# Optimization experiments

Measured on AMD Instinct MI355X. Metric: run time of the kernel, lower is better.

## Reference

```python
import math
import jax, jax.numpy as jnp
import numpy as np

NUM_HEADS = 16
HEAD_DIM = 128
CTX = 4096

def _rope_tables(head_dim, context_length, theta_base=10000.0):
    inv_freq = 1.0 / (theta_base ** (np.arange(0, head_dim, 2)[: head_dim // 2].astype(np.float32) / head_dim))
    pos = np.arange(context_length, dtype=np.float32)
    ang = pos[:, None] * inv_freq[None, :]
    ang = np.concatenate([ang, ang], axis=1)  # [ctx, head_dim]
    return jnp.asarray(np.cos(ang), jnp.float32), jnp.asarray(np.sin(ang), jnp.float32)

def _apply_rope(x, cos, sin):
    # x: [b, h, s, d]
    s, d = x.shape[2], x.shape[3]
    x1, x2 = x[..., : d // 2], x[..., d // 2 :]
    rotated = jnp.concatenate([-x2, x1], axis=-1)
    c = cos[:s][None, None]
    sn = sin[:s][None, None]
    return x * c + rotated * sn

def setup_inputs() -> dict:
    key = jax.random.key(0)
    kx, kq, kk, kv, ko = jax.random.split(key, 5)
    B, S, H = 2, 2048, 2048
    scale = 1.0 / math.sqrt(H)
    x = jax.random.normal(kx, (B, S, H), jnp.float32)
    Wq = jax.random.normal(kq, (H, H), jnp.float32) * scale
    Wk = jax.random.normal(kk, (H, H), jnp.float32) * scale
    Wv = jax.random.normal(kv, (H, H), jnp.float32) * scale
    Wo = jax.random.normal(ko, (H, H), jnp.float32) * scale
    cos, sin = _rope_tables(HEAD_DIM, CTX)
    return {"x": x, "Wq": Wq, "Wk": Wk, "Wv": Wv, "Wo": Wo, "cos": cos, "sin": sin}

def reference(x, Wq, Wk, Wv, Wo, cos, sin):
    B, S, Hd = x.shape
    nh, hd = NUM_HEADS, HEAD_DIM
    # nn.Linear(no bias): y = x @ W.T
    q = jnp.einsum('bsh,oh->bso', x, Wq).reshape(B, S, nh, hd).transpose(0, 2, 1, 3)
    k = jnp.einsum('bsh,oh->bso', x, Wk).reshape(B, S, nh, hd).transpose(0, 2, 1, 3)
    v = jnp.einsum('bsh,oh->bso', x, Wv).reshape(B, S, nh, hd).transpose(0, 2, 1, 3)
    q = _apply_rope(q, cos, sin)
    k = _apply_rope(k, cos, sin)
    # NOTE: faithful to source bug: scores are divided by (1/sqrt(d)),
    # i.e. MULTIPLIED by sqrt(head_dim).
    scores = jnp.einsum('bhqd,bhkd->bhqk', q, k) * math.sqrt(hd)
    causal = jnp.triu(jnp.ones((S, S), bool), k=1)
    scores = jnp.where(causal[None, None], -jnp.inf, scores)
    attn = jax.nn.softmax(scores, axis=-1)
    ctx = jnp.einsum('bhqk,bhkd->bhqd', attn, v)
    ctx = ctx.transpose(0, 2, 1, 3).reshape(B, S, Hd)
    return jnp.einsum('bsh,oh->bso', ctx, Wo)
```

## Files before the change

kernel.cpp:

```cpp
#include <hip/hip_runtime.h>

typedef unsigned short u16;
typedef __attribute__((ext_vector_type(8))) _Float16 f16x8;
typedef __attribute__((ext_vector_type(4))) float f32x4;

#define S_CTX 2048
#define DMODEL 2048

#define WAITVM(N) asm volatile("s_waitcnt vmcnt(" #N ")" ::: "memory")
#define SBAR() __builtin_amdgcn_s_barrier()

__device__ __forceinline__ u16 f2h(float f) {
  _Float16 h = (_Float16)f; u16 u; __builtin_memcpy(&u, &h, 2); return u;
}
__device__ __forceinline__ float h2f(u16 u) {
  _Float16 h; __builtin_memcpy(&h, &u, 2); return (float)h;
}
__device__ __forceinline__ void gload16(const u16* g, u16* l) {
  __builtin_amdgcn_global_load_lds(
      (const __attribute__((address_space(1))) unsigned int*)g,
      (__attribute__((address_space(3))) unsigned int*)l, 16, 0, 0);
}

__global__ void split_all(const float* __restrict__ x, const float* __restrict__ Wq,
                          const float* __restrict__ Wk, const float* __restrict__ Wv,
                          const float* __restrict__ Wo,
                          u16* xh, u16* xl, u16* Wqh, u16* Wql,
                          u16* Wkh, u16* Wkl, u16* Wvh, u16* Woh) {
  size_t i = (size_t)blockIdx.x * 256 + threadIdx.x;
  const size_t NX = 8388608, NW = 4194304;
  if (i < NX) {
    float v = x[i];
    u16 h = f2h(v);
    xh[i] = h; xl[i] = f2h(v - h2f(h));
  } else {
    size_t j = i - NX;
    int wsel = (int)(j >> 22);
    size_t o = j & (NW - 1);
    if (wsel == 0) { float v = Wq[o] * 64.f; u16 h = f2h(v); Wqh[o] = h; Wql[o] = f2h(v - h2f(h)); }
    else if (wsel == 1) { float v = Wk[o] * 64.f; u16 h = f2h(v); Wkh[o] = h; Wkl[o] = f2h(v - h2f(h)); }
    else if (wsel == 2) { Wvh[o] = f2h(Wv[o] * 64.f); }
    else { Woh[o] = f2h(Wo[o] * 64.f); }
  }
}

template <int NT, int MODE>
__device__ __forceinline__ void gemm_core(
    u16* sm, const u16* __restrict__ Am, const u16* __restrict__ Alm,
    const u16* __restrict__ Bm, const u16* __restrict__ Blm,
    float* __restrict__ Cf, u16* __restrict__ Ch,
    const float* __restrict__ cosT, const float* __restrict__ sinT,
    int N, int K, int m0, int n0, float oscale) {
  const int tid = threadIdx.x;
  const int w = tid >> 6, lane = tid & 63;
  const int quad = lane >> 4, l16 = lane & 15;
  const int wm = (w >> 1) << 6, wn = (w & 1) << 6;
  const int lrow = lane >> 2, lcol = (lane & 3) << 3;
  const int lcs = lcol ^ (((lrow >> 1) & 3) << 3);
  const int qsw = (quad << 3) ^ (((l16 >> 1) & 3) << 3);

  auto stageH = [&](int bufb, int k0) {
#pragma unroll
    for (int j = 0; j < 2; ++j) {
      int r = w * 32 + j * 16 + lrow;
      int lb = bufb + (w * 32 + j * 16) * 32;
      size_t ga = (size_t)(m0 + r) * K + k0 + lcs;
      size_t gb = (size_t)(n0 + r) * K + k0 + lcs;
      gload16(Am + ga, &sm[lb]);
      gload16(Bm + gb, &sm[lb + 4096]);
    }
  };
  auto stageL = [&](int bufb, int k0) {
#pragma unroll
    for (int j = 0; j < 2; ++j) {
      int r = w * 32 + j * 16 + lrow;
      int lb = bufb + (w * 32 + j * 16) * 32;
      size_t ga = (size_t)(m0 + r) * K + k0 + lcs;
      size_t gb = (size_t)(n0 + r) * K + k0 + lcs;
      gload16(Blm + gb, &sm[lb + 8192]);
      gload16(Alm + ga, &sm[lb + 12288]);
    }
  };

  f32x4 acc[4][4];
#pragma unroll
  for (int i = 0; i < 4; ++i)
#pragma unroll
    for (int n = 0; n < 4; ++n) acc[i][n] = (f32x4){0.f, 0.f, 0.f, 0.f};

  const int NTL = K >> 5;

  if (NT == 3) {
    stageH(0, 0);
    stageL(0, 0);
    for (int t = 0; t < NTL; ++t) {
      const int cur = (t & 1) << 14;
      const int nxt = 16384 - cur;
      const int k0n = (t + 1) << 5;
      const bool more = (t + 1 < NTL);

      WAITVM(4);
      SBAR();
      f16x8 ah[4], bh[4];
#pragma unroll
      for (int i = 0; i < 4; ++i)
        ah[i] = *(const f16x8*)&sm[cur + (wm + i * 16 + l16) * 32 + qsw];
#pragma unroll
      for (int n = 0; n < 4; ++n)
        bh[n] = *(const f16x8*)&sm[cur + 4096 + (wn + n * 16 + l16) * 32 + qsw];
      if (more) stageH(nxt, k0n);
#pragma unroll
      for (int i = 0; i < 4; ++i)
#pragma unroll
        for (int n = 0; n < 4; ++n)
          acc[i][n] = __builtin_amdgcn_mfma_f32_16x16x32_f16(ah[i], bh[n], acc[i][n], 0, 0, 0);

      if (more) { WAITVM(4); } else { WAITVM(0); }
      SBAR();
      f16x8 bl[4], al[4];
#pragma unroll
      for (int n = 0; n < 4; ++n)
        bl[n] = *(const f16x8*)&sm[cur + 8192 + (wn + n * 16 + l16) * 32 + qsw];
#pragma unroll
      for (int i = 0; i < 4; ++i)
        al[i] = *(const f16x8*)&sm[cur + 12288 + (wm + i * 16 + l16) * 32 + qsw];
      if (more) stageL(nxt, k0n);
#pragma unroll
      for (int i = 0; i < 4; ++i)
#pragma unroll
        for (int n = 0; n < 4; ++n) {
          acc[i][n] = __builtin_amdgcn_mfma_f32_16x16x32_f16(ah[i], bl[n], acc[i][n], 0, 0, 0);
          acc[i][n] = __builtin_amdgcn_mfma_f32_16x16x32_f16(al[i], bh[n], acc[i][n], 0, 0, 0);
        }
    }
  } else {
    stageH(0, 0);
    stageH(8192, 32);
    for (int t = 0; t < NTL; ++t) {
      const int cur = (t % 3) * 8192;
      if (t + 1 < NTL) { WAITVM(4); } else { WAITVM(0); }
      SBAR();
      f16x8 ah[4], bh[4];
#pragma unroll
      for (int i = 0; i < 4; ++i)
        ah[i] = *(const f16x8*)&sm[cur + (wm + i * 16 + l16) * 32 + qsw];
#pragma unroll
      for (int n = 0; n < 4; ++n)
        bh[n] = *(const f16x8*)&sm[cur + 4096 + (wn + n * 16 + l16) * 32 + qsw];
      if (t + 2 < NTL) stageH(((t + 2) % 3) * 8192, (t + 2) << 5);
#pragma unroll
      for (int i = 0; i < 4; ++i)
#pragma unroll
        for (int n = 0; n < 4; ++n)
          acc[i][n] = __builtin_amdgcn_mfma_f32_16x16x32_f16(ah[i], bh[n], acc[i][n], 0, 0, 0);
    }
  }

  if (MODE == 3) {
    float* fs = (float*)sm;
    const int p = w >> 1;
#pragma unroll
    for (int i = 0; i < 4; ++i) {
      __syncthreads();
#pragma unroll
      for (int n = 0; n < 4; ++n)
#pragma unroll
        for (int r = 0; r < 4; ++r)
          fs[p * 2048 + (quad * 4 + r) * 128 + wn + n * 16 + l16] = acc[i][n][r];
      __syncthreads();
#pragma unroll
      for (int n = 0; n < 4; ++n) {
        const int col = wn + n * 16 + l16;
        const int cc = col ^ 64;
        const float sgn = (col < 64) ? -1.f : 1.f;
#pragma unroll
        for (int r = 0; r < 4; ++r) {
          const int row16 = quad * 4 + r;
          const int grow = m0 + wm + i * 16 + row16;
          const int s = grow & (S_CTX - 1);
          const float c = cosT[s * 128 + col];
          const float sn = sinT[s * 128 + col];
          const float x = fs[p * 2048 + row16 * 128 + col];
          const float xp = fs[p * 2048 + row16 * 128 + cc];
          Ch[(size_t)grow * N + n0 + col] = f2h((x * c + sgn * xp * sn) * oscale);
        }
      }
    }
    return;
  }
#pragma unroll
  for (int i = 0; i < 4; ++i)
#pragma unroll
    for (int n = 0; n < 4; ++n) {
      const int row0 = m0 + wm + i * 16 + quad * 4;
      const int col = n0 + wn + n * 16 + l16;
      if (MODE == 0) {
#pragma unroll
        for (int r = 0; r < 4; ++r) Cf[(size_t)(row0 + r) * N + col] = acc[i][n][r] * oscale;
      } else {
        int brow = row0 >> 11, s0 = row0 & 2047;
        int hh = col >> 7, d = col & 127;
        ushort4 pk;
        pk.x = f2h(acc[i][n][0]);
        pk.y = f2h(acc[i][n][1]);
        pk.z = f2h(acc[i][n][2]);
        pk.w = f2h(acc[i][n][3]);
        *(ushort4*)(Ch + ((size_t)(brow * 16 + hh) * 128 + d) * 2048 + s0) = pk;
      }
    }
}

__global__ __launch_bounds__(256) void qkv_kernel(
    const u16* __restrict__ xh, const u16* __restrict__ xl,
    const u16* __restrict__ Wqh, const u16* __restrict__ Wql,
    const u16* __restrict__ Wkh, const u16* __restrict__ Wkl,
    const u16* __restrict__ Wvh,
    const float* __restrict__ cosT, const float* __restrict__ sinT,
    u16* qh, u16* kh, u16* vt) {
  __shared__ u16 sm[32768];
  const int m0 = blockIdx.y << 7, n0 = blockIdx.x << 7;
  const float qs = 0.002762135864009951f;
  if (blockIdx.z == 0)
    gemm_core<3, 3>(sm, xh, xl, Wqh, Wql, nullptr, qh, cosT, sinT, DMODEL, DMODEL, m0, n0, qs);
  else if (blockIdx.z == 1)
    gemm_core<3, 3>(sm, xh, xl, Wkh, Wkl, nullptr, kh, cosT, sinT, DMODEL, DMODEL, m0, n0, 1.f);
  else
    gemm_core<1, 2>(sm, xh, nullptr, Wvh, nullptr, nullptr, vt, nullptr, nullptr, DMODEL, DMODEL, m0, n0, 1.f);
}

__global__ __launch_bounds__(256) void out_kernel(
    const u16* __restrict__ ch, const u16* __restrict__ Woh, float* __restrict__ out) {
  __shared__ u16 sm[24576];
  gemm_core<1, 0>(sm, ch, nullptr, Woh, nullptr, out, nullptr, nullptr, nullptr, DMODEL, DMODEL,
                  blockIdx.y << 7, blockIdx.x << 7, 1.f / 4096.f);
}

__global__ __launch_bounds__(512, 4) void attn_kernel(
    const u16* __restrict__ Qh, const u16* __restrict__ Kh,
    const u16* __restrict__ VT, u16* __restrict__ Ch) {
  const int lin = blockIdx.x | (blockIdx.y << 4);
  const int pair = lin & 255;
  const int bh = pair >> 3;
  const int q8 = pair & 7;
  const int qt = (lin < 256) ? (15 - q8) : q8;
  const int b = bh >> 4, h = bh & 15;
  const int tid = threadIdx.x;
  const int w = tid >> 6, lane = tid & 63;
  const int quad = lane >> 4, l16 = lane & 15;

  __shared__ u16 sKh[64 * 136];
  __shared__ u16 sVt[128 * 72];
  __shared__ u16 sPb[8 * 1088];
  u16* sP = &sPb[w * 1088];

  const size_t bhbase = (size_t)b * S_CTX * DMODEL + (size_t)h * 128;
  const size_t vtbase = (size_t)bh * 128 * 2048;

  int kr[2], kc[2], vr[2], vc[2];
#pragma unroll
  for (int j = 0; j < 2; ++j) {
    int c = j * 512 + tid;
    kr[j] = c >> 4; kc[j] = (c & 15) << 3;
    vr[j] = c >> 3; vc[j] = (c & 7) << 3;
  }

  const int qr0 = qt * 128 + w * 16;
  const size_t qoff = bhbase + (size_t)(qr0 + l16) * DMODEL;
  f16x8 qf[4];
#pragma unroll
  for (int c = 0; c < 4; ++c) qf[c] = *(const f16x8*)(Qh + qoff + c * 32 + quad * 8);

  f32x4 oacc[8];
#pragma unroll
  for (int d = 0; d < 8; ++d) oacc[d] = (f32x4){0.f, 0.f, 0.f, 0.f};
  float m_r = -INFINITY;
  float l_r = 0.f;

  f16x8 rkh[2], rvt[2];
#pragma unroll
  for (int j = 0; j < 2; ++j) {
    rkh[j] = *(const f16x8*)(Kh + bhbase + (size_t)kr[j] * DMODEL + kc[j]);
    rvt[j] = *(const f16x8*)(VT + vtbase + (size_t)vr[j] * 2048 + vc[j]);
  }

  const int nkt = 2 * qt + 2;
  for (int kt = 0; kt < nkt; ++kt) {
    __syncthreads();
#pragma unroll
    for (int j = 0; j < 2; ++j) {
      *(f16x8*)&sKh[kr[j] * 136 + kc[j]] = rkh[j];
      *(f16x8*)&sVt[vr[j] * 72 + vc[j]] = rvt[j];
    }
    __syncthreads();
    if (kt + 1 < nkt) {
#pragma unroll
      for (int j = 0; j < 2; ++j) {
        size_t g = bhbase + (size_t)((kt + 1) * 64 + kr[j]) * DMODEL + kc[j];
        rkh[j] = *(const f16x8*)(Kh + g);
        rvt[j] = *(const f16x8*)(VT + vtbase + (size_t)vr[j] * 2048 + (kt + 1) * 64 + vc[j]);
      }
    }

    const bool active = (kt * 64) <= (qr0 + 15);
    if (active) {
      f32x4 sacc[4];
#pragma unroll
      for (int n = 0; n < 4; ++n) sacc[n] = (f32x4){0.f, 0.f, 0.f, 0.f};
      __builtin_amdgcn_s_setprio(1);
#pragma unroll
      for (int n = 0; n < 4; ++n)
#pragma unroll
        for (int c = 0; c < 4; ++c) {
          f16x8 kf = *(const f16x8*)&sKh[(n * 16 + l16) * 136 + c * 32 + quad * 8];
          sacc[n] = __builtin_amdgcn_mfma_f32_16x16x32_f16(kf, qf[c], sacc[n], 0, 0, 0);
        }
      __builtin_amdgcn_s_setprio(0);

      const int qi = qr0 + l16;
      const int kb = kt * 64 + quad * 4;
      float pm[4][4];
      float rmax = -INFINITY;
#pragma unroll
      for (int n = 0; n < 4; ++n)
#pragma unroll
        for (int r = 0; r < 4; ++r) {
          float sc = sacc[n][r];
          if (kb + n * 16 + r > qi) sc = -INFINITY;
          pm[n][r] = sc;
          rmax = fmaxf(rmax, sc);
        }
      rmax = fmaxf(rmax, __shfl_xor(rmax, 16, 64));
      rmax = fmaxf(rmax, __shfl_xor(rmax, 32, 64));

      const float mnew = fmaxf(m_r, rmax);
      const float alpha = __expf(m_r - mnew);
      m_r = mnew;
      l_r *= alpha;
      float rsum = 0.f;
#pragma unroll
      for (int n = 0; n < 4; ++n)
#pragma unroll
        for (int r = 0; r < 4; ++r) {
          float pv = __expf(pm[n][r] - m_r);
          pm[n][r] = pv;
          rsum += pv;
        }
      rsum += __shfl_xor(rsum, 16, 64);
      rsum += __shfl_xor(rsum, 32, 64);
      l_r += rsum;

      float apv[4];
#pragma unroll
      for (int r = 0; r < 4; ++r)
        apv[r] = __shfl(alpha, (lane & 48) | (quad * 4 + r), 64);
#pragma unroll
      for (int d = 0; d < 8; ++d)
#pragma unroll
        for (int r = 0; r < 4; ++r) oacc[d][r] *= apv[r];

#pragma unroll
      for (int n = 0; n < 4; ++n) {
        ushort4 pk;
        pk.x = f2h(pm[n][0]);
        pk.y = f2h(pm[n][1]);
        pk.z = f2h(pm[n][2]);
        pk.w = f2h(pm[n][3]);
        *(ushort4*)&sP[l16 * 68 + n * 16 + quad * 4] = pk;
      }

      __builtin_amdgcn_s_setprio(1);
#pragma unroll
      for (int c = 0; c < 2; ++c) {
        f16x8 pf = *(const f16x8*)&sP[l16 * 68 + c * 32 + quad * 8];
#pragma unroll
        for (int d = 0; d < 8; ++d) {
          f16x8 vf = *(const f16x8*)&sVt[(d * 16 + l16) * 72 + c * 32 + quad * 8];
          oacc[d] = __builtin_amdgcn_mfma_f32_16x16x32_f16(pf, vf, oacc[d], 0, 0, 0);
        }
      }
      __builtin_amdgcn_s_setprio(0);
    }
  }

  const float invl = 1.f / l_r;
  float ipv[4];
#pragma unroll
  for (int r = 0; r < 4; ++r)
    ipv[r] = __shfl(invl, (lane & 48) | (quad * 4 + r), 64);
#pragma unroll
  for (int d = 0; d < 8; ++d)
#pragma unroll
    for (int r = 0; r < 4; ++r) {
      int row = qr0 + quad * 4 + r;
      Ch[bhbase + (size_t)row * DMODEL + d * 16 + l16] = f2h(oacc[d][r] * ipv[r]);
    }
}

extern "C" void kernel_launch(void* const* d_in, const int* in_sizes, int n_in,
                              void* d_out, int out_size, void* d_ws, size_t ws_size,
                              hipStream_t stream) {
  const float* x    = (const float*)d_in[0];
  const float* Wq   = (const float*)d_in[1];
  const float* Wk   = (const float*)d_in[2];
  const float* Wv   = (const float*)d_in[3];
  const float* Wo   = (const float*)d_in[4];
  const float* cosT = (const float*)d_in[5];
  const float* sinT = (const float*)d_in[6];
  float* out = (float*)d_out;

  const size_t NX = 8388608;
  const size_t NW = 4194304;
  u16* p = (u16*)d_ws;
  u16* xh  = p; p += NX;  u16* xl  = p; p += NX;
  u16* Wqh = p; p += NW;  u16* Wql = p; p += NW;
  u16* Wkh = p; p += NW;  u16* Wkl = p; p += NW;
  u16* Wvh = p; p += NW;  u16* Woh = p; p += NW;
  u16* qh  = p; p += NX;  u16* kh  = p; p += NX;
  u16* vt  = p; p += NX;
  u16* ch  = p; p += NX;

  split_all<<<98304, 256, 0, stream>>>(x, Wq, Wk, Wv, Wo,
                                       xh, xl, Wqh, Wql, Wkh, Wkl, Wvh, Woh);

  qkv_kernel<<<dim3(16, 32, 3), 256, 0, stream>>>(xh, xl, Wqh, Wql, Wkh, Wkl, Wvh,
                                                  cosT, sinT, qh, kh, vt);

  attn_kernel<<<dim3(16, 32), 512, 0, stream>>>(qh, kh, vt, ch);

  out_kernel<<<dim3(16, 32), 256, 0, stream>>>(ch, Woh, out);
}
```

Measured before the change: 539.8 us.

## Fuse Q, K, V projections into one 768-thread block sharing the x tile

The QKV projection no longer launches three separate 256-thread blocks per output tile, one each for Q, K and V. It now launches one 768-thread block with three wave groups that share a single staged tile of x (high and low halves) in LDS and each compute Q, K or V. This removes redundant global loads of the activation tile and cuts the block count. In exchange, LDS per block rises to about 112KB and blocks are larger, so occupancy drops. The V group also idles during the low-precision correction phase and the RoPE epilogue.

```diff
diff --git a/kernel.cpp b/kernel.cpp
--- a/kernel.cpp
+++ b/kernel.cpp
@@ -70,60 +70,128 @@
       gload16(Bm + gb, &sm[lb + 4096]);
     }
   };
+
+  f32x4 acc[4][4];
+#pragma unroll
+  for (int i = 0; i < 4; ++i)
+#pragma unroll
+    for (int n = 0; n < 4; ++n) acc[i][n] = (f32x4){0.f, 0.f, 0.f, 0.f};
+
+  const int NTL = K >> 5;
+
+  stageH(0, 0);
+  stageH(8192, 32);
+  for (int t = 0; t < NTL; ++t) {
+    const int cur = (t % 3) * 8192;
+    if (t + 1 < NTL) { WAITVM(4); } else { WAITVM(0); }
+    SBAR();
+    f16x8 ah[4], bh[4];
+#pragma unroll
+    for (int i = 0; i < 4; ++i)
+      ah[i] = *(const f16x8*)&sm[cur + (wm + i * 16 + l16) * 32 + qsw];
+#pragma unroll
+    for (int n = 0; n < 4; ++n)
+      bh[n] = *(const f16x8*)&sm[cur + 4096 + (wn + n * 16 + l16) * 32 + qsw];
+    if (t + 2 < NTL) stageH(((t + 2) % 3) * 8192, (t + 2) << 5);
+#pragma unroll
+    for (int i = 0; i < 4; ++i)
+#pragma unroll
+      for (int n = 0; n < 4; ++n)
+        acc[i][n] = __builtin_amdgcn_mfma_f32_16x16x32_f16(ah[i], bh[n], acc[i][n], 0, 0, 0);
+  }
+
+#pragma unroll
+  for (int i = 0; i < 4; ++i)
+#pragma unroll
+    for (int n = 0; n < 4; ++n) {
+      const int row0 = m0 + wm + i * 16 + quad * 4;
+      const int col = n0 + wn + n * 16 + l16;
+#pragma unroll
+      for (int r = 0; r < 4; ++r) Cf[(size_t)(row0 + r) * N + col] = acc[i][n][r] * oscale;
+    }
+}
+
+__global__ __launch_bounds__(768) void qkv_kernel(
+    const u16* __restrict__ xh, const u16* __restrict__ xl,
+    const u16* __restrict__ Wqh, const u16* __restrict__ Wql,
+    const u16* __restrict__ Wkh, const u16* __restrict__ Wkl,
+    const u16* __restrict__ Wvh,
+    const float* __restrict__ cosT, const float* __restrict__ sinT,
+    u16* qh, u16* kh, u16* vt) {
+  __shared__ u16 sm[57344];
+  const int tid = threadIdx.x;
+  const int w = tid >> 6, lane = tid & 63;
+  const int grp = w >> 2, wl = w & 3;
+  const int quad = lane >> 4, l16 = lane & 15;
+  const int wm = (wl >> 1) << 6, wn = (wl & 1) << 6;
+  const int m0 = blockIdx.y << 7, n0 = blockIdx.x << 7;
+
+  const int lcs = ((tid & 3) << 3) ^ (((tid >> 3) & 3) << 3);
+  const int qsw = (quad << 3) ^ (((l16 >> 1) & 3) << 3);
+  const int tid8 = tid << 3;
+  const size_t aoff = (size_t)(m0 + ((tid >> 2) & 127)) * 2048 + lcs;
+  const size_t boff = (size_t)(n0 + ((tid >> 2) & 127)) * 2048 + lcs;
+  const bool stg = (tid < 512);
+
+  auto stageH = [&](int bufb, int k0) {
+    if (stg) {
+      gload16(xh + aoff + k0, &sm[bufb + tid8]);
+      gload16(Wqh + boff + k0, &sm[bufb + 8192 + tid8]);
+      gload16(Wkh + boff + k0, &sm[bufb + 12288 + tid8]);
+      gload16(Wvh + boff + k0, &sm[bufb + 16384 + tid8]);
+    }
+  };
   auto stageL = [&](int bufb, int k0) {
-#pragma unroll
-    for (int j = 0; j < 2; ++j) {
-      int r = w * 32 + j * 16 + lrow;
-      int lb = bufb + (w * 32 + j * 16) * 32;
-      size_t ga = (size_t)(m0 + r) * K + k0 + lcs;
-      size_t gb = (size_t)(n0 + r) * K + k0 + lcs;
-      gload16(Blm + gb, &sm[lb + 8192]);
-      gload16(Alm + ga, &sm[lb + 12288]);
+    if (stg) {
+      gload16(xl + aoff + k0, &sm[bufb + 4096 + tid8]);
+      gload16(Wql + boff + k0, &sm[bufb + 20480 + tid8]);
+      gload16(Wkl + boff + k0, &sm[bufb + 24576 + tid8]);
     }
   };
 
+  const int bBh = 8192 + (grp << 12);
+  const int bBl = 20480 + (grp << 12);
+
   f32x4 acc[4][4];
 #pragma unroll
   for (int i = 0; i < 4; ++i)
 #pragma unroll
     for (int n = 0; n < 4; ++n) acc[i][n] = (f32x4){0.f, 0.f, 0.f, 0.f};
 
-  const int NTL = K >> 5;
-
-  if (NT == 3) {
-    stageH(0, 0);
-    stageL(0, 0);
-    for (int t = 0; t < NTL; ++t) {
-      const int cur = (t & 1) << 14;
-      const int nxt = 16384 - cur;
-      const int k0n = (t + 1) << 5;
-      const bool more = (t + 1 < NTL);
-
-      WAITVM(4);
-      SBAR();
-      f16x8 ah[4], bh[4];
+  stageH(0, 0);
+  stageL(0, 0);
+  for (int t = 0; t < 64; ++t) {
+    const int cur = (t & 1) ? 28672 : 0;
+    const int nxt = 28672 - cur;
+    const int k0n = (t + 1) << 5;
+    const bool more = (t + 1 < 64);
+
+    WAITVM(3);
+    SBAR();
+    f16x8 ah[4], bh[4];
+#pragma unroll
+    for (int i = 0; i < 4; ++i)
+      ah[i] = *(const f16x8*)&sm[cur + (wm + i * 16 + l16) * 32 + qsw];
+#pragma unroll
+    for (int n = 0; n < 4; ++n)
+      bh[n] = *(const f16x8*)&sm[cur + bBh + (wn + n * 16 + l16) * 32 + qsw];
+    if (more) stageH(nxt, k0n);
+#pragma unroll
+    for (int i = 0; i < 4; ++i)
+#pragma unroll
+      for (int n = 0; n < 4; ++n)
+        acc[i][n] = __builtin_amdgcn_mfma_f32_16x16x32_f16(ah[i], bh[n], acc[i][n], 0, 0, 0);
+
+    if (more) { WAITVM(4); } else { WAITVM(0); }
+    SBAR();
+    if (grp < 2) {
+      f16x8 bl[4], al[4];
+#pragma unroll
+      for (int n = 0; n < 4; ++n)
+        bl[n] = *(const f16x8*)&sm[cur + bBl + (wn + n * 16 + l16) * 32 + qsw];
 #pragma unroll
       for (int i = 0; i < 4; ++i)
-        ah[i] = *(const f16x8*)&sm[cur + (wm + i * 16 + l16) * 32 + qsw];
-#pragma unroll
-      for (int n = 0; n < 4; ++n)
-        bh[n] = *(const f16x8*)&sm[cur + 4096 + (wn + n * 16 + l16) * 32 + qsw];
-      if (more) stageH(nxt, k0n);
-#pragma unroll
-      for (int i = 0; i < 4; ++i)
-#pragma unroll
-        for (int n = 0; n < 4; ++n)
-          acc[i][n] = __builtin_amdgcn_mfma_f32_16x16x32_f16(ah[i], bh[n], acc[i][n], 0, 0, 0);
-
-      if (more) { WAITVM(4); } else { WAITVM(0); }
-      SBAR();
-      f16x8 bl[4], al[4];
-#pragma unroll
-      for (int n = 0; n < 4; ++n)
-        bl[n] = *(const f16x8*)&sm[cur + 8192 + (wn + n * 16 + l16) * 32 + qsw];
-#pragma unroll
-      for (int i = 0; i < 4; ++i)
-        al[i] = *(const f16x8*)&sm[cur + 12288 + (wm + i * 16 + l16) * 32 + qsw];
+        al[i] = *(const f16x8*)&sm[cur + 4096 + (wm + i * 16 + l16) * 32 + qsw];
       if (more) stageL(nxt, k0n);
 #pragma unroll
       for (int i = 0; i < 4; ++i)
@@ -132,42 +200,45 @@
           acc[i][n] = __builtin_amdgcn_mfma_f32_16x16x32_f16(ah[i], bl[n], acc[i][n], 0, 0, 0);
           acc[i][n] = __builtin_amdgcn_mfma_f32_16x16x32_f16(al[i], bh[n], acc[i][n], 0, 0, 0);
         }
-    }
-  } else {
-    stageH(0, 0);
-    stageH(8192, 32);
-    for (int t = 0; t < NTL; ++t) {
-      const int cur = (t % 3) * 8192;
-      if (t + 1 < NTL) { WAITVM(4); } else { WAITVM(0); }
-      SBAR();
-      f16x8 ah[4], bh[4];
-#pragma unroll
-      for (int i = 0; i < 4; ++i)
-        ah[i] = *(const f16x8*)&sm[cur + (wm + i * 16 + l16) * 32 + qsw];
-#pragma unroll
-      for (int n = 0; n < 4; ++n)
-        bh[n] = *(const f16x8*)&sm[cur + 4096 + (wn + n * 16 + l16) * 32 + qsw];
-      if (t + 2 < NTL) stageH(((t + 2) % 3) * 8192, (t + 2) << 5);
-#pragma unroll
-      for (int i = 0; i < 4; ++i)
-#pragma unroll
-        for (int n = 0; n < 4; ++n)
-          acc[i][n] = __builtin_amdgcn_mfma_f32_16x16x32_f16(ah[i], bh[n], acc[i][n], 0, 0, 0);
-    }
-  }
-
-  if (MODE == 3) {
-    float* fs = (float*)sm;
-    const int p = w >> 1;
-#pragma unroll
-    for (int i = 0; i < 4; ++i) {
-      __syncthreads();
+    } else {
+      if (more) stageL(nxt, k0n);
+    }
+  }
+
+  if (grp == 2) {
+#pragma unroll
+    for (int i = 0; i < 4; ++i)
+#pragma unroll
+      for (int n = 0; n < 4; ++n) {
+        const int row0 = m0 + wm + i * 16 + quad * 4;
+        const int col = n0 + wn + n * 16 + l16;
+        int brow = row0 >> 11, s0 = row0 & 2047;
+        int hh = col >> 7, d = col & 127;
+        ushort4 pk;
+        pk.x = f2h(acc[i][n][0]);
+        pk.y = f2h(acc[i][n][1]);
+        pk.z = f2h(acc[i][n][2]);
+        pk.w = f2h(acc[i][n][3]);
+        *(ushort4*)(vt + ((size_t)(brow * 16 + hh) * 128 + d) * 2048 + s0) = pk;
+      }
+  }
+
+  u16* Ch = (grp == 1) ? kh : qh;
+  const float oscale = (grp == 1) ? 1.f : 0.002762135864009951f;
+  float* fs = (float*)sm;
+  const int p = w >> 1;
+#pragma unroll
+  for (int i = 0; i < 4; ++i) {
+    __syncthreads();
+    if (grp < 2) {
 #pragma unroll
       for (int n = 0; n < 4; ++n)
 #pragma unroll
         for (int r = 0; r < 4; ++r)
           fs[p * 2048 + (quad * 4 + r) * 128 + wn + n * 16 + l16] = acc[i][n][r];
-      __syncthreads();
+    }
+    __syncthreads();
+    if (grp < 2) {
 #pragma unroll
       for (int n = 0; n < 4; ++n) {
         const int col = wn + n * 16 + l16;
@@ -182,50 +253,11 @@
           const float sn = sinT[s * 128 + col];
           const float x = fs[p * 2048 + row16 * 128 + col];
           const float xp = fs[p * 2048 + row16 * 128 + cc];
-          Ch[(size_t)grow * N + n0 + col] = f2h((x * c + sgn * xp * sn) * oscale);
+          Ch[(size_t)grow * DMODEL + n0 + col] = f2h((x * c + sgn * xp * sn) * oscale);
         }
       }
     }
-    return;
-  }
-#pragma unroll
-  for (int i = 0; i < 4; ++i)
-#pragma unroll
-    for (int n = 0; n < 4; ++n) {
-      const int row0 = m0 + wm + i * 16 + quad * 4;
-      const int col = n0 + wn + n * 16 + l16;
-      if (MODE == 0) {
-#pragma unroll
-        for (int r = 0; r < 4; ++r) Cf[(size_t)(row0 + r) * N + col] = acc[i][n][r] * oscale;
-      } else {
-        int brow = row0 >> 11, s0 = row0 & 2047;
-        int hh = col >> 7, d = col & 127;
-        ushort4 pk;
-        pk.x = f2h(acc[i][n][0]);
-        pk.y = f2h(acc[i][n][1]);
-        pk.z = f2h(acc[i][n][2]);
-        pk.w = f2h(acc[i][n][3]);
-        *(ushort4*)(Ch + ((size_t)(brow * 16 + hh) * 128 + d) * 2048 + s0) = pk;
-      }
-    }
-}
-
-__global__ __launch_bounds__(256) void qkv_kernel(
-    const u16* __restrict__ xh, const u16* __restrict__ xl,
-    const u16* __restrict__ Wqh, const u16* __restrict__ Wql,
-    const u16* __restrict__ Wkh, const u16* __restrict__ Wkl,
-    const u16* __restrict__ Wvh,
-    const float* __restrict__ cosT, const float* __restrict__ sinT,
-    u16* qh, u16* kh, u16* vt) {
-  __shared__ u16 sm[32768];
-  const int m0 = blockIdx.y << 7, n0 = blockIdx.x << 7;
-  const float qs = 0.002762135864009951f;
-  if (blockIdx.z == 0)
-    gemm_core<3, 3>(sm, xh, xl, Wqh, Wql, nullptr, qh, cosT, sinT, DMODEL, DMODEL, m0, n0, qs);
-  else if (blockIdx.z == 1)
-    gemm_core<3, 3>(sm, xh, xl, Wkh, Wkl, nullptr, kh, cosT, sinT, DMODEL, DMODEL, m0, n0, 1.f);
-  else
-    gemm_core<1, 2>(sm, xh, nullptr, Wvh, nullptr, nullptr, vt, nullptr, nullptr, DMODEL, DMODEL, m0, n0, 1.f);
+  }
 }
 
 __global__ __launch_bounds__(256) void out_kernel(
@@ -422,8 +454,8 @@
   split_all<<<98304, 256, 0, stream>>>(x, Wq, Wk, Wv, Wo,
                                        xh, xl, Wqh, Wql, Wkh, Wkl, Wvh, Woh);
 
-  qkv_kernel<<<dim3(16, 32, 3), 256, 0, stream>>>(xh, xl, Wqh, Wql, Wkh, Wkl, Wvh,
-                                                  cosT, sinT, qh, kh, vt);
+  qkv_kernel<<<dim3(16, 32), 768, 0, stream>>>(xh, xl, Wqh, Wql, Wkh, Wkl, Wvh,
+                                               cosT, sinT, qh, kh, vt);
 
   attn_kernel<<<dim3(16, 32), 512, 0, stream>>>(qh, kh, vt, ch);
 
```

After: 498.4 us. 7.7% less time.
